# Performance work log

Measured on AMD Instinct MI355X. Metric: run time of the kernel, lower is better.

## Reference

```python
import jax, jax.numpy as jnp
import numpy as np

THRESHOLD = 1.0

@jax.custom_vjp
def spike(u):
    # Heaviside fire with snntorch ATan surrogate gradient (alpha=2.0)
    return (u > 0).astype(u.dtype)

def _spike_fwd(u):
    return spike(u), u

def _spike_bwd(u, g):
    # d/du atan surrogate: (alpha/2) / (1 + (pi/2*alpha*u)^2) with alpha=2 -> 1/(1+(pi*u)^2)
    return (g / (1.0 + (jnp.pi * u) ** 2),)

spike.defvjp(_spike_fwd, _spike_bwd)


def setup_inputs() -> dict:
    key = jax.random.key(0)
    k1, k2, k3, k4 = jax.random.split(key, 4)
    B, D, M = 1024, 256, 256
    x = jax.random.normal(k1, (B, D), dtype=jnp.float32)
    mem_states = jax.random.normal(k2, (M, B, D), dtype=jnp.float32)
    # mode_selector Linear(D -> M)
    W = jax.random.normal(k3, (M, D), dtype=jnp.float32) / np.sqrt(D)
    b = jax.random.normal(k4, (M,), dtype=jnp.float32) * 0.01
    return {"x": x, "mem_states": mem_states, "W": W, "b": b}


def reference(x, mem_states, W, b):
    M = mem_states.shape[0]
    # gating scores: [B, M]
    mode_scores = jax.nn.softmax(x @ W.T + b, axis=-1)
    # snn.Leaky(beta=i) for i in range(M): beta is the integer loop index
    betas = jnp.arange(M, dtype=x.dtype)[:, None, None]  # [M,1,1]
    # subtract-reset uses detached spike of the incoming membrane
    reset = jax.lax.stop_gradient((mem_states - THRESHOLD > 0).astype(x.dtype))
    mem_new = betas * mem_states + x[None, :, :] - reset * THRESHOLD  # [M,B,D]
    spk = spike(mem_new - THRESHOLD)  # [M,B,D]
    # faithful to source broadcast: [M,B,D] * [1,B,M] (requires D == M), sum over modes
    mixed = (spk * mode_scores[None, :, :]).sum(axis=0)  # [B,D]
    return mixed, mem_new, mode_scores
```

## Files before the change

### kernel.cpp

```cpp
#include <hip/hip_runtime.h>

#define THRESH 1.0f

typedef float fvec4 __attribute__((ext_vector_type(4)));

__global__ __launch_bounds__(256) void transpose_kernel(
    const float* __restrict__ W, float* __restrict__ Wt, int M, int D)
{
    __shared__ float tile[32][33];
    const int tilesK = D / 32;
    const int bx = blockIdx.x % tilesK;
    const int by = blockIdx.x / tilesK;
    const int lx = threadIdx.x & 31;
    const int ly = threadIdx.x >> 5;
    #pragma unroll
    for (int j = 0; j < 4; ++j)
        tile[ly + j * 8][lx] = W[(size_t)(by * 32 + ly + j * 8) * D + bx * 32 + lx];
    __syncthreads();
    #pragma unroll
    for (int j = 0; j < 4; ++j)
        Wt[(size_t)(bx * 32 + ly + j * 8) * M + by * 32 + lx] = tile[lx][ly + j * 8];
}

__global__ __launch_bounds__(256) void mega_kernel(
    const float* __restrict__ x, const float* __restrict__ mem,
    const float* __restrict__ Wt, const float* __restrict__ bias,
    float* __restrict__ mem_new, float* __restrict__ scores,
    float* __restrict__ mixed, int plane4)
{
    const int b    = blockIdx.x;
    const int tid  = threadIdx.x;
    const int wave = tid >> 6;
    const int lane = tid & 63;

    __shared__ __align__(16) float x_lds[256];
    __shared__ fvec4 sc_lds[64];
    __shared__ fvec4 cnt_lds[4][64];

    x_lds[tid] = x[(size_t)b * 256 + tid];
    __syncthreads();

    if (wave == 0) {
        const fvec4* Wt4 = reinterpret_cast<const fvec4*>(Wt);
        fvec4 acc = {0.f, 0.f, 0.f, 0.f};
        #pragma unroll 4
        for (int k = 0; k < 256; ++k) {
            const fvec4 w = Wt4[(size_t)k * 64 + lane];
            const float xk = x_lds[k];
            acc.x = fmaf(w.x, xk, acc.x);
            acc.y = fmaf(w.y, xk, acc.y);
            acc.z = fmaf(w.z, xk, acc.z);
            acc.w = fmaf(w.w, xk, acc.w);
        }
        const fvec4 bv = reinterpret_cast<const fvec4*>(bias)[lane];
        fvec4 lg;
        lg.x = acc.x + bv.x; lg.y = acc.y + bv.y;
        lg.z = acc.z + bv.z; lg.w = acc.w + bv.w;

        float mx = fmaxf(fmaxf(lg.x, lg.y), fmaxf(lg.z, lg.w));
        #pragma unroll
        for (int off = 32; off; off >>= 1) mx = fmaxf(mx, __shfl_xor(mx, off, 64));

        fvec4 e;
        e.x = expf(lg.x - mx); e.y = expf(lg.y - mx);
        e.z = expf(lg.z - mx); e.w = expf(lg.w - mx);
        float s = (e.x + e.y) + (e.z + e.w);
        #pragma unroll
        for (int off = 32; off; off >>= 1) s += __shfl_xor(s, off, 64);

        fvec4 sc;
        sc.x = e.x / s; sc.y = e.y / s; sc.z = e.z / s; sc.w = e.w / s;
        sc_lds[lane] = sc;
        reinterpret_cast<fvec4*>(scores)[(size_t)b * 64 + lane] = sc;
    }

    const int idx4 = b * 64 + lane;
    const fvec4 xv = reinterpret_cast<const fvec4*>(x_lds)[lane];
    const fvec4* mem4 = reinterpret_cast<const fvec4*>(mem);
    fvec4* out4       = reinterpret_cast<fvec4*>(mem_new);

    float cx = 0.f, cy = 0.f, cz = 0.f, cw = 0.f;
    const int m0 = wave * 64;

    #pragma unroll 4
    for (int j = 0; j < 64; ++j) {
        const int m = m0 + j;
        const float bm = (float)m;
        const size_t off = (size_t)m * plane4 + idx4;
        const fvec4 mv = __builtin_nontemporal_load(&mem4[off]);

        fvec4 nv;
        nv.x = __fsub_rn(__fadd_rn(__fmul_rn(bm, mv.x), xv.x),
                         (mv.x - THRESH > 0.f) ? THRESH : 0.f);
        nv.y = __fsub_rn(__fadd_rn(__fmul_rn(bm, mv.y), xv.y),
                         (mv.y - THRESH > 0.f) ? THRESH : 0.f);
        nv.z = __fsub_rn(__fadd_rn(__fmul_rn(bm, mv.z), xv.z),
                         (mv.z - THRESH > 0.f) ? THRESH : 0.f);
        nv.w = __fsub_rn(__fadd_rn(__fmul_rn(bm, mv.w), xv.w),
                         (mv.w - THRESH > 0.f) ? THRESH : 0.f);

        __builtin_nontemporal_store(nv, &out4[off]);

        cx += (nv.x - THRESH > 0.f) ? 1.f : 0.f;
        cy += (nv.y - THRESH > 0.f) ? 1.f : 0.f;
        cz += (nv.z - THRESH > 0.f) ? 1.f : 0.f;
        cw += (nv.w - THRESH > 0.f) ? 1.f : 0.f;
    }
    fvec4 cv; cv.x = cx; cv.y = cy; cv.z = cz; cv.w = cw;
    cnt_lds[wave][lane] = cv;
    __syncthreads();

    if (wave == 0) {
        const fvec4 c0 = cnt_lds[0][lane];
        const fvec4 c1 = cnt_lds[1][lane];
        const fvec4 c2 = cnt_lds[2][lane];
        const fvec4 c3 = cnt_lds[3][lane];
        fvec4 c;
        c.x = (c0.x + c1.x) + (c2.x + c3.x);
        c.y = (c0.y + c1.y) + (c2.y + c3.y);
        c.z = (c0.z + c1.z) + (c2.z + c3.z);
        c.w = (c0.w + c1.w) + (c2.w + c3.w);
        const fvec4 sc = sc_lds[lane];
        fvec4 r;
        r.x = sc.x * c.x; r.y = sc.y * c.y;
        r.z = sc.z * c.z; r.w = sc.w * c.w;
        reinterpret_cast<fvec4*>(mixed)[(size_t)idx4] = r;
    }
}

__global__ __launch_bounds__(256) void scores_kernel_fb(
    const float* __restrict__ x, const float* __restrict__ W,
    const float* __restrict__ bias, float* __restrict__ scores,
    int D, int M)
{
    const int b = blockIdx.x;
    __shared__ __align__(16) float x_lds[256];
    __shared__ float logits[256];
    __shared__ float wred[4];
    const int tid  = threadIdx.x;
    const int wave = tid >> 6;
    const int lane = tid & 63;
    x_lds[tid] = x[(size_t)b * D + tid];
    __syncthreads();
    const float4* W4 = reinterpret_cast<const float4*>(W);
    const float4  xv = reinterpret_cast<const float4*>(x_lds)[lane];
    for (int i = 0; i < 64; ++i) {
        const int m = wave * 64 + i;
        const float4 wv = W4[(size_t)m * 64 + lane];
        float p = wv.x * xv.x + wv.y * xv.y + wv.z * xv.z + wv.w * xv.w;
        #pragma unroll
        for (int off = 32; off; off >>= 1) p += __shfl_xor(p, off, 64);
        if (lane == 0) logits[m] = p + bias[m];
    }
    __syncthreads();
    float l = logits[tid];
    float mx = l;
    #pragma unroll
    for (int off = 32; off; off >>= 1) mx = fmaxf(mx, __shfl_xor(mx, off, 64));
    if (lane == 0) wred[wave] = mx;
    __syncthreads();
    mx = fmaxf(fmaxf(wred[0], wred[1]), fmaxf(wred[2], wred[3]));
    __syncthreads();
    const float e = expf(l - mx);
    float s = e;
    #pragma unroll
    for (int off = 32; off; off >>= 1) s += __shfl_xor(s, off, 64);
    if (lane == 0) wred[wave] = s;
    __syncthreads();
    const float tot = wred[0] + wred[1] + wred[2] + wred[3];
    scores[(size_t)b * M + tid] = e / tot;
}

__global__ __launch_bounds__(256) void neuron_kernel_fb(
    const float* __restrict__ x, const float* __restrict__ mem,
    const float* __restrict__ scores, float* __restrict__ mixed,
    float* __restrict__ mem_new, int M, int plane4)
{
    const int idx = blockIdx.x * 256 + threadIdx.x;
    if (idx >= plane4) return;
    const float4* x4   = reinterpret_cast<const float4*>(x);
    const float4* mem4 = reinterpret_cast<const float4*>(mem);
    const float4* sc4  = reinterpret_cast<const float4*>(scores);
    float4* out4       = reinterpret_cast<float4*>(mem_new);
    float4* mix4       = reinterpret_cast<float4*>(mixed);
    const float4 xv = x4[idx];
    float cx = 0.f, cy = 0.f, cz = 0.f, cw = 0.f;
    #pragma unroll 4
    for (int m = 0; m < M; ++m) {
        const float bm = (float)m;
        const size_t off = (size_t)m * plane4 + idx;
        const float4 mv = mem4[off];
        float4 nv;
        nv.x = __fsub_rn(__fadd_rn(__fmul_rn(bm, mv.x), xv.x),
                         (mv.x - THRESH > 0.f) ? THRESH : 0.f);
        nv.y = __fsub_rn(__fadd_rn(__fmul_rn(bm, mv.y), xv.y),
                         (mv.y - THRESH > 0.f) ? THRESH : 0.f);
        nv.z = __fsub_rn(__fadd_rn(__fmul_rn(bm, mv.z), xv.z),
                         (mv.z - THRESH > 0.f) ? THRESH : 0.f);
        nv.w = __fsub_rn(__fadd_rn(__fmul_rn(bm, mv.w), xv.w),
                         (mv.w - THRESH > 0.f) ? THRESH : 0.f);
        out4[off] = nv;
        cx += (nv.x - THRESH > 0.f) ? 1.f : 0.f;
        cy += (nv.y - THRESH > 0.f) ? 1.f : 0.f;
        cz += (nv.z - THRESH > 0.f) ? 1.f : 0.f;
        cw += (nv.w - THRESH > 0.f) ? 1.f : 0.f;
    }
    const float4 sc = sc4[idx];
    float4 mx;
    mx.x = sc.x * cx; mx.y = sc.y * cy; mx.z = sc.z * cz; mx.w = sc.w * cw;
    mix4[idx] = mx;
}

extern "C" void kernel_launch(void* const* d_in, const int* in_sizes, int n_in,
                              void* d_out, int out_size, void* d_ws, size_t ws_size,
                              hipStream_t stream) {
    const float* x    = (const float*)d_in[0];
    const float* mem  = (const float*)d_in[1];
    const float* W    = (const float*)d_in[2];
    const float* bias = (const float*)d_in[3];

    const int M = in_sizes[3];
    const int D = in_sizes[2] / M;
    const int B = in_sizes[0] / D;
    const int plane  = B * D;
    const int plane4 = plane / 4;

    float* out_mixed  = (float*)d_out;
    float* out_mem    = out_mixed + plane;
    float* out_scores = out_mem + (size_t)M * plane;

    const size_t wt_bytes = (size_t)M * D * sizeof(float);

    const bool shapes_ok = (D == 256) && (M == 256);

    if (shapes_ok && ws_size >= wt_bytes) {
        float* Wt = (float*)d_ws;
        transpose_kernel<<<(M / 32) * (D / 32), 256, 0, stream>>>(W, Wt, M, D);
        mega_kernel<<<B, 256, 0, stream>>>(
            x, mem, Wt, bias, out_mem, out_scores, out_mixed, plane4);
    } else {
        scores_kernel_fb<<<B, 256, 0, stream>>>(x, W, bias, out_scores, D, M);
        neuron_kernel_fb<<<(plane4 + 255) / 256, 256, 0, stream>>>(
            x, mem, out_scores, out_mixed, out_mem, M, plane4);
    }
}
```

Baseline: 111.7 us.

## Process two batch rows per block and spread scores GEMV across all waves

Each block now handles two batch rows, with all 256 threads computing one logit each for both rows. Each W element loaded is reused for two rows, and x values are broadcast through readlane instead of LDS. This replaces the single-wave GEMV that left three waves idle. The streaming loop is split into two halves of 128 modes over 128 float4 positions, which halves the grid and lengthens each thread's loop. The costs are fewer blocks (512), an extra block-level softmax reduction with syncs, and a changed fallback grid size.

```diff
diff --git a/kernel.cpp b/kernel.cpp
--- a/kernel.cpp
+++ b/kernel.cpp
@@ -3,6 +3,10 @@
 #define THRESH 1.0f
 
 typedef float fvec4 __attribute__((ext_vector_type(4)));
+
+__device__ __forceinline__ float rl(float v, int l) {
+    return __int_as_float(__builtin_amdgcn_readlane(__float_as_int(v), l));
+}
 
 __global__ __launch_bounds__(256) void transpose_kernel(
     const float* __restrict__ W, float* __restrict__ Wt, int M, int D)
@@ -22,71 +26,89 @@
         Wt[(size_t)(bx * 32 + ly + j * 8) * M + by * 32 + lx] = tile[lx][ly + j * 8];
 }
 
-__global__ __launch_bounds__(256) void mega_kernel(
+__global__ __launch_bounds__(256) void rowpair_kernel(
     const float* __restrict__ x, const float* __restrict__ mem,
     const float* __restrict__ Wt, const float* __restrict__ bias,
     float* __restrict__ mem_new, float* __restrict__ scores,
     float* __restrict__ mixed, int plane4)
 {
-    const int b    = blockIdx.x;
+    const int b0   = blockIdx.x * 2;
     const int tid  = threadIdx.x;
     const int wave = tid >> 6;
     const int lane = tid & 63;
 
-    __shared__ __align__(16) float x_lds[256];
-    __shared__ fvec4 sc_lds[64];
-    __shared__ fvec4 cnt_lds[4][64];
-
-    x_lds[tid] = x[(size_t)b * 256 + tid];
-    __syncthreads();
-
-    if (wave == 0) {
-        const fvec4* Wt4 = reinterpret_cast<const fvec4*>(Wt);
-        fvec4 acc = {0.f, 0.f, 0.f, 0.f};
-        #pragma unroll 4
-        for (int k = 0; k < 256; ++k) {
-            const fvec4 w = Wt4[(size_t)k * 64 + lane];
-            const float xk = x_lds[k];
-            acc.x = fmaf(w.x, xk, acc.x);
-            acc.y = fmaf(w.y, xk, acc.y);
-            acc.z = fmaf(w.z, xk, acc.z);
-            acc.w = fmaf(w.w, xk, acc.w);
-        }
-        const fvec4 bv = reinterpret_cast<const fvec4*>(bias)[lane];
-        fvec4 lg;
-        lg.x = acc.x + bv.x; lg.y = acc.y + bv.y;
-        lg.z = acc.z + bv.z; lg.w = acc.w + bv.w;
-
-        float mx = fmaxf(fmaxf(lg.x, lg.y), fmaxf(lg.z, lg.w));
-        #pragma unroll
-        for (int off = 32; off; off >>= 1) mx = fmaxf(mx, __shfl_xor(mx, off, 64));
-
-        fvec4 e;
-        e.x = expf(lg.x - mx); e.y = expf(lg.y - mx);
-        e.z = expf(lg.z - mx); e.w = expf(lg.w - mx);
-        float s = (e.x + e.y) + (e.z + e.w);
-        #pragma unroll
-        for (int off = 32; off; off >>= 1) s += __shfl_xor(s, off, 64);
-
-        fvec4 sc;
-        sc.x = e.x / s; sc.y = e.y / s; sc.z = e.z / s; sc.w = e.w / s;
-        sc_lds[lane] = sc;
-        reinterpret_cast<fvec4*>(scores)[(size_t)b * 64 + lane] = sc;
-    }
-
-    const int idx4 = b * 64 + lane;
-    const fvec4 xv = reinterpret_cast<const fvec4*>(x_lds)[lane];
+    __shared__ __align__(16) float sc_lds[2][256];
+    __shared__ fvec4 cnt_lds[2][128];
+    __shared__ float wredm[2][4];
+    __shared__ float wreds[2][4];
+
+    const fvec4 xq0 = reinterpret_cast<const fvec4*>(x)[(size_t)b0 * 64 + lane];
+    const fvec4 xq1 = reinterpret_cast<const fvec4*>(x)[(size_t)(b0 + 1) * 64 + lane];
+
+    float a0 = 0.f, a1 = 0.f;
+    #pragma unroll 4
+    for (int j = 0; j < 64; ++j) {
+        const float w0 = Wt[(size_t)(4 * j + 0) * 256 + tid];
+        const float w1 = Wt[(size_t)(4 * j + 1) * 256 + tid];
+        const float w2 = Wt[(size_t)(4 * j + 2) * 256 + tid];
+        const float w3 = Wt[(size_t)(4 * j + 3) * 256 + tid];
+        a0 = fmaf(w0, rl(xq0.x, j), a0);
+        a0 = fmaf(w1, rl(xq0.y, j), a0);
+        a0 = fmaf(w2, rl(xq0.z, j), a0);
+        a0 = fmaf(w3, rl(xq0.w, j), a0);
+        a1 = fmaf(w0, rl(xq1.x, j), a1);
+        a1 = fmaf(w1, rl(xq1.y, j), a1);
+        a1 = fmaf(w2, rl(xq1.z, j), a1);
+        a1 = fmaf(w3, rl(xq1.w, j), a1);
+    }
+    const float bv = bias[tid];
+    const float l0 = a0 + bv, l1 = a1 + bv;
+
+    float m0 = l0, m1 = l1;
+    #pragma unroll
+    for (int off = 32; off; off >>= 1) {
+        m0 = fmaxf(m0, __shfl_xor(m0, off, 64));
+        m1 = fmaxf(m1, __shfl_xor(m1, off, 64));
+    }
+    if (lane == 0) { wredm[0][wave] = m0; wredm[1][wave] = m1; }
+    __syncthreads();
+    m0 = fmaxf(fmaxf(wredm[0][0], wredm[0][1]), fmaxf(wredm[0][2], wredm[0][3]));
+    m1 = fmaxf(fmaxf(wredm[1][0], wredm[1][1]), fmaxf(wredm[1][2], wredm[1][3]));
+
+    const float e0 = expf(l0 - m0), e1 = expf(l1 - m1);
+    float s0 = e0, s1 = e1;
+    #pragma unroll
+    for (int off = 32; off; off >>= 1) {
+        s0 += __shfl_xor(s0, off, 64);
+        s1 += __shfl_xor(s1, off, 64);
+    }
+    if (lane == 0) { wreds[0][wave] = s0; wreds[1][wave] = s1; }
+    __syncthreads();
+    const float t0 = wreds[0][0] + wreds[0][1] + wreds[0][2] + wreds[0][3];
+    const float t1 = wreds[1][0] + wreds[1][1] + wreds[1][2] + wreds[1][3];
+
+    const float sc0 = e0 / t0, sc1 = e1 / t1;
+    sc_lds[0][tid] = sc0;
+    sc_lds[1][tid] = sc1;
+    scores[(size_t)b0 * 256 + tid]       = sc0;
+    scores[(size_t)(b0 + 1) * 256 + tid] = sc1;
+
+    const int h = tid >> 7;
+    const int p = tid & 127;
+    const int pos4 = b0 * 64 + p;
+    const fvec4 xv = reinterpret_cast<const fvec4*>(x)[pos4];
+
     const fvec4* mem4 = reinterpret_cast<const fvec4*>(mem);
     fvec4* out4       = reinterpret_cast<fvec4*>(mem_new);
 
     float cx = 0.f, cy = 0.f, cz = 0.f, cw = 0.f;
-    const int m0 = wave * 64;
-
-    #pragma unroll 4
-    for (int j = 0; j < 64; ++j) {
-        const int m = m0 + j;
+    const int mstart = h * 128;
+
+    #pragma unroll 8
+    for (int mm = 0; mm < 128; ++mm) {
+        const int m = mstart + mm;
         const float bm = (float)m;
-        const size_t off = (size_t)m * plane4 + idx4;
+        const size_t off = (size_t)m * plane4 + pos4;
         const fvec4 mv = __builtin_nontemporal_load(&mem4[off]);
 
         fvec4 nv;
@@ -107,24 +129,19 @@
         cw += (nv.w - THRESH > 0.f) ? 1.f : 0.f;
     }
     fvec4 cv; cv.x = cx; cv.y = cy; cv.z = cz; cv.w = cw;
-    cnt_lds[wave][lane] = cv;
-    __syncthreads();
-
-    if (wave == 0) {
-        const fvec4 c0 = cnt_lds[0][lane];
-        const fvec4 c1 = cnt_lds[1][lane];
-        const fvec4 c2 = cnt_lds[2][lane];
-        const fvec4 c3 = cnt_lds[3][lane];
-        fvec4 c;
-        c.x = (c0.x + c1.x) + (c2.x + c3.x);
-        c.y = (c0.y + c1.y) + (c2.y + c3.y);
-        c.z = (c0.z + c1.z) + (c2.z + c3.z);
-        c.w = (c0.w + c1.w) + (c2.w + c3.w);
-        const fvec4 sc = sc_lds[lane];
+    cnt_lds[h][p] = cv;
+    __syncthreads();
+
+    if (h == 0) {
+        const fvec4 cA = cnt_lds[0][p];
+        const fvec4 cB = cnt_lds[1][p];
+        const fvec4 sc = reinterpret_cast<const fvec4*>(sc_lds[p >> 6])[p & 63];
         fvec4 r;
-        r.x = sc.x * c.x; r.y = sc.y * c.y;
-        r.z = sc.z * c.z; r.w = sc.w * c.w;
-        reinterpret_cast<fvec4*>(mixed)[(size_t)idx4] = r;
+        r.x = sc.x * (cA.x + cB.x);
+        r.y = sc.y * (cA.y + cB.y);
+        r.z = sc.z * (cA.z + cB.z);
+        r.w = sc.w * (cA.w + cB.w);
+        reinterpret_cast<fvec4*>(mixed)[pos4] = r;
     }
 }
 
@@ -231,16 +248,16 @@
 
     const size_t wt_bytes = (size_t)M * D * sizeof(float);
 
-    const bool shapes_ok = (D == 256) && (M == 256);
+    const bool shapes_ok = (D == 256) && (M == 256) && (B % 2 == 0);
 
     if (shapes_ok && ws_size >= wt_bytes) {
         float* Wt = (float*)d_ws;
         transpose_kernel<<<(M / 32) * (D / 32), 256, 0, stream>>>(W, Wt, M, D);
-        mega_kernel<<<B, 256, 0, stream>>>(
+        rowpair_kernel<<<B / 2, 256, 0, stream>>>(
             x, mem, Wt, bias, out_mem, out_scores, out_mixed, plane4);
     } else {
         scores_kernel_fb<<<B, 256, 0, stream>>>(x, W, bias, out_scores, D, M);
-        neuron_kernel_fb<<<(plane4 + 255) / 256, 256, 0, stream>>>(
+        neuron_kernel_fb<<<(plane + 255) / 256 / 4, 256, 0, stream>>>(
             x, mem, out_scores, out_mixed, out_mem, M, plane4);
     }
 }
```

Measured after the change: 106.7 us. 1.05x faster.

## Spread gating GEMV across all waves and stagger it against streaming loop

Applied to the files above, without the earlier changes.

The softmax gating matvec, previously computed by a single wave while the other three waited, is now split so every thread computes one logit, using readlane broadcasts of x and block-wide max/sum reductions. Alternating groups of blocks run this prologue either before the mem_states stream or halfway through it, so compute phases in different blocks interleave with memory traffic. The goal is to shorten the serial compute head and overlap it with bandwidth-bound streaming. The cost is extra block-wide barriers in the middle of the streaming loop and a larger unroll, which may raise register pressure.

```diff
diff --git a/kernel.cpp b/kernel.cpp
--- a/kernel.cpp
+++ b/kernel.cpp
@@ -3,6 +3,10 @@
 #define THRESH 1.0f
 
 typedef float fvec4 __attribute__((ext_vector_type(4)));
+
+__device__ __forceinline__ float rl(float v, int l) {
+    return __int_as_float(__builtin_amdgcn_readlane(__float_as_int(v), l));
+}
 
 __global__ __launch_bounds__(256) void transpose_kernel(
     const float* __restrict__ W, float* __restrict__ Wt, int M, int D)
@@ -22,7 +26,7 @@
         Wt[(size_t)(bx * 32 + ly + j * 8) * M + by * 32 + lx] = tile[lx][ly + j * 8];
 }
 
-__global__ __launch_bounds__(256) void mega_kernel(
+__global__ __launch_bounds__(256) void row_kernel(
     const float* __restrict__ x, const float* __restrict__ mem,
     const float* __restrict__ Wt, const float* __restrict__ bias,
     float* __restrict__ mem_new, float* __restrict__ scores,
@@ -32,63 +36,25 @@
     const int tid  = threadIdx.x;
     const int wave = tid >> 6;
     const int lane = tid & 63;
-
-    __shared__ __align__(16) float x_lds[256];
-    __shared__ fvec4 sc_lds[64];
+    const int q    = wave;
+    const int p    = lane;
+    const int pos4 = b * 64 + p;
+
+    __shared__ __align__(16) float sc_f[256];
     __shared__ fvec4 cnt_lds[4][64];
-
-    x_lds[tid] = x[(size_t)b * 256 + tid];
-    __syncthreads();
-
-    if (wave == 0) {
-        const fvec4* Wt4 = reinterpret_cast<const fvec4*>(Wt);
-        fvec4 acc = {0.f, 0.f, 0.f, 0.f};
-        #pragma unroll 4
-        for (int k = 0; k < 256; ++k) {
-            const fvec4 w = Wt4[(size_t)k * 64 + lane];
-            const float xk = x_lds[k];
-            acc.x = fmaf(w.x, xk, acc.x);
-            acc.y = fmaf(w.y, xk, acc.y);
-            acc.z = fmaf(w.z, xk, acc.z);
-            acc.w = fmaf(w.w, xk, acc.w);
-        }
-        const fvec4 bv = reinterpret_cast<const fvec4*>(bias)[lane];
-        fvec4 lg;
-        lg.x = acc.x + bv.x; lg.y = acc.y + bv.y;
-        lg.z = acc.z + bv.z; lg.w = acc.w + bv.w;
-
-        float mx = fmaxf(fmaxf(lg.x, lg.y), fmaxf(lg.z, lg.w));
-        #pragma unroll
-        for (int off = 32; off; off >>= 1) mx = fmaxf(mx, __shfl_xor(mx, off, 64));
-
-        fvec4 e;
-        e.x = expf(lg.x - mx); e.y = expf(lg.y - mx);
-        e.z = expf(lg.z - mx); e.w = expf(lg.w - mx);
-        float s = (e.x + e.y) + (e.z + e.w);
-        #pragma unroll
-        for (int off = 32; off; off >>= 1) s += __shfl_xor(s, off, 64);
-
-        fvec4 sc;
-        sc.x = e.x / s; sc.y = e.y / s; sc.z = e.z / s; sc.w = e.w / s;
-        sc_lds[lane] = sc;
-        reinterpret_cast<fvec4*>(scores)[(size_t)b * 64 + lane] = sc;
-    }
-
-    const int idx4 = b * 64 + lane;
-    const fvec4 xv = reinterpret_cast<const fvec4*>(x_lds)[lane];
+    __shared__ float wredm[4];
+    __shared__ float wreds[4];
+
     const fvec4* mem4 = reinterpret_cast<const fvec4*>(mem);
     fvec4* out4       = reinterpret_cast<fvec4*>(mem_new);
+    const fvec4 xv    = reinterpret_cast<const fvec4*>(x)[pos4];
 
     float cx = 0.f, cy = 0.f, cz = 0.f, cw = 0.f;
-    const int m0 = wave * 64;
-
-    #pragma unroll 4
-    for (int j = 0; j < 64; ++j) {
-        const int m = m0 + j;
+
+    auto step = [&](int m) {
         const float bm = (float)m;
-        const size_t off = (size_t)m * plane4 + idx4;
+        const size_t off = (size_t)m * plane4 + pos4;
         const fvec4 mv = __builtin_nontemporal_load(&mem4[off]);
-
         fvec4 nv;
         nv.x = __fsub_rn(__fadd_rn(__fmul_rn(bm, mv.x), xv.x),
                          (mv.x - THRESH > 0.f) ? THRESH : 0.f);
@@ -98,33 +64,82 @@
                          (mv.z - THRESH > 0.f) ? THRESH : 0.f);
         nv.w = __fsub_rn(__fadd_rn(__fmul_rn(bm, mv.w), xv.w),
                          (mv.w - THRESH > 0.f) ? THRESH : 0.f);
-
         __builtin_nontemporal_store(nv, &out4[off]);
-
         cx += (nv.x - THRESH > 0.f) ? 1.f : 0.f;
         cy += (nv.y - THRESH > 0.f) ? 1.f : 0.f;
         cz += (nv.z - THRESH > 0.f) ? 1.f : 0.f;
         cw += (nv.w - THRESH > 0.f) ? 1.f : 0.f;
-    }
+    };
+
+    auto prologue = [&]() {
+        const fvec4 xq = reinterpret_cast<const fvec4*>(x)[(size_t)b * 64 + lane];
+        float a0 = 0.f;
+        #pragma unroll 4
+        for (int j = 0; j < 64; ++j) {
+            const float w0 = Wt[(size_t)(4 * j + 0) * 256 + tid];
+            const float w1 = Wt[(size_t)(4 * j + 1) * 256 + tid];
+            const float w2 = Wt[(size_t)(4 * j + 2) * 256 + tid];
+            const float w3 = Wt[(size_t)(4 * j + 3) * 256 + tid];
+            a0 = fmaf(w0, rl(xq.x, j), a0);
+            a0 = fmaf(w1, rl(xq.y, j), a0);
+            a0 = fmaf(w2, rl(xq.z, j), a0);
+            a0 = fmaf(w3, rl(xq.w, j), a0);
+        }
+        const float l = a0 + bias[tid];
+
+        float mx = l;
+        #pragma unroll
+        for (int off = 32; off; off >>= 1) mx = fmaxf(mx, __shfl_xor(mx, off, 64));
+        if (lane == 0) wredm[wave] = mx;
+        __syncthreads();
+        mx = fmaxf(fmaxf(wredm[0], wredm[1]), fmaxf(wredm[2], wredm[3]));
+
+        const float e = expf(l - mx);
+        float s = e;
+        #pragma unroll
+        for (int off = 32; off; off >>= 1) s += __shfl_xor(s, off, 64);
+        if (lane == 0) wreds[wave] = s;
+        __syncthreads();
+        const float tot = wreds[0] + wreds[1] + wreds[2] + wreds[3];
+
+        const float sc = e / tot;
+        sc_f[tid] = sc;
+        scores[(size_t)b * 256 + tid] = sc;
+    };
+
+    const int mstart = q * 64;
+
+    if (((blockIdx.x >> 3) & 1) == 0) {
+        #pragma unroll 8
+        for (int m = mstart; m < mstart + 32; ++m) step(m);
+        prologue();
+        #pragma unroll 8
+        for (int m = mstart + 32; m < mstart + 64; ++m) step(m);
+    } else {
+        prologue();
+        #pragma unroll 8
+        for (int m = mstart; m < mstart + 64; ++m) step(m);
+    }
+
     fvec4 cv; cv.x = cx; cv.y = cy; cv.z = cz; cv.w = cw;
-    cnt_lds[wave][lane] = cv;
-    __syncthreads();
-
-    if (wave == 0) {
-        const fvec4 c0 = cnt_lds[0][lane];
-        const fvec4 c1 = cnt_lds[1][lane];
-        const fvec4 c2 = cnt_lds[2][lane];
-        const fvec4 c3 = cnt_lds[3][lane];
+    cnt_lds[q][p] = cv;
+    __syncthreads();
+
+    if (q == 0) {
+        const fvec4 c0 = cnt_lds[0][p];
+        const fvec4 c1 = cnt_lds[1][p];
+        const fvec4 c2 = cnt_lds[2][p];
+        const fvec4 c3 = cnt_lds[3][p];
         fvec4 c;
         c.x = (c0.x + c1.x) + (c2.x + c3.x);
         c.y = (c0.y + c1.y) + (c2.y + c3.y);
         c.z = (c0.z + c1.z) + (c2.z + c3.z);
         c.w = (c0.w + c1.w) + (c2.w + c3.w);
-        const fvec4 sc = sc_lds[lane];
+        const fvec4 sc = reinterpret_cast<const fvec4*>(sc_f)[p];
         fvec4 r;
         r.x = sc.x * c.x; r.y = sc.y * c.y;
         r.z = sc.z * c.z; r.w = sc.w * c.w;
-        reinterpret_cast<fvec4*>(mixed)[(size_t)idx4] = r;
+        reinterpret_cast<fvec4*>(mixed)[pos4] = r;
     }
 }
 
@@ -147,10 +162,10 @@
     for (int i = 0; i < 64; ++i) {
         const int m = wave * 64 + i;
         const float4 wv = W4[(size_t)m * 64 + lane];
-        float p = wv.x * xv.x + wv.y * xv.y + wv.z * xv.z + wv.w * xv.w;
+        float pp = wv.x * xv.x + wv.y * xv.y + wv.z * xv.z + wv.w * xv.w;
         #pragma unroll
-        for (int off = 32; off; off >>= 1) p += __shfl_xor(p, off, 64);
-        if (lane == 0) logits[m] = p + bias[m];
+        for (int off = 32; off; off >>= 1) pp += __shfl_xor(pp, off, 64);
+        if (lane == 0) logits[m] = pp + bias[m];
     }
     __syncthreads();
     float l = logits[tid];
@@ -236,7 +251,7 @@
     if (shapes_ok && ws_size >= wt_bytes) {
         float* Wt = (float*)d_ws;
         transpose_kernel<<<(M / 32) * (D / 32), 256, 0, stream>>>(W, Wt, M, D);
-        mega_kernel<<<B, 256, 0, stream>>>(
+        row_kernel<<<B, 256, 0, stream>>>(
             x, mem, Wt, bias, out_mem, out_scores, out_mixed, plane4);
     } else {
         scores_kernel_fb<<<B, 256, 0, stream>>>(x, W, bias, out_scores, D, M);
```

Result: slower. 121.5 us (+8.8%).

## Process two batch rows per 512-thread block with uneven mode split

Applied to the files above, without the earlier changes.

Replaces the one-row-per-block kernel with a 512-thread block that handles two batch rows. Two waves compute the gating softmax, one per row, broadcasting x with readlane instead of staging it in LDS. Four thread groups split the 256 modes into uneven ranges (46/70/70/70), so the group that also did the GEMV gets fewer modes. The aim is to balance the GEMV work against the streaming loop and to halve the number of blocks and barriers, at the cost of more registers per block and a hardcoded partition.

```diff
diff --git a/kernel.cpp b/kernel.cpp
--- a/kernel.cpp
+++ b/kernel.cpp
@@ -3,6 +3,10 @@
 #define THRESH 1.0f
 
 typedef float fvec4 __attribute__((ext_vector_type(4)));
+
+__device__ __forceinline__ float rl(float v, int l) {
+    return __int_as_float(__builtin_amdgcn_readlane(__float_as_int(v), l));
+}
 
 __global__ __launch_bounds__(256) void transpose_kernel(
     const float* __restrict__ W, float* __restrict__ Wt, int M, int D)
@@ -22,35 +26,58 @@
         Wt[(size_t)(bx * 32 + ly + j * 8) * M + by * 32 + lx] = tile[lx][ly + j * 8];
 }
 
-__global__ __launch_bounds__(256) void mega_kernel(
+__global__ __launch_bounds__(512, 4) void rowpair512b_kernel(
     const float* __restrict__ x, const float* __restrict__ mem,
     const float* __restrict__ Wt, const float* __restrict__ bias,
     float* __restrict__ mem_new, float* __restrict__ scores,
     float* __restrict__ mixed, int plane4)
 {
-    const int b    = blockIdx.x;
+    const int b0   = blockIdx.x * 2;
     const int tid  = threadIdx.x;
     const int wave = tid >> 6;
     const int lane = tid & 63;
-
-    __shared__ __align__(16) float x_lds[256];
-    __shared__ fvec4 sc_lds[64];
-    __shared__ fvec4 cnt_lds[4][64];
-
-    x_lds[tid] = x[(size_t)b * 256 + tid];
-    __syncthreads();
-
-    if (wave == 0) {
+    const int q    = tid >> 7;
+    const int pp   = tid & 127;
+    const int pos4 = b0 * 64 + pp;
+
+    __shared__ fvec4 sc_lds[2][64];
+    __shared__ fvec4 cnt_lds[4][128];
+
+    const fvec4* mem4 = reinterpret_cast<const fvec4*>(mem);
+    fvec4* out4       = reinterpret_cast<fvec4*>(mem_new);
+    const fvec4* x4   = reinterpret_cast<const fvec4*>(x);
+
+    if (wave < 2) {
+        const int row = b0 + wave;
         const fvec4* Wt4 = reinterpret_cast<const fvec4*>(Wt);
+        const fvec4 xq = x4[(size_t)row * 64 + lane];
         fvec4 acc = {0.f, 0.f, 0.f, 0.f};
         #pragma unroll 4
-        for (int k = 0; k < 256; ++k) {
-            const fvec4 w = Wt4[(size_t)k * 64 + lane];
-            const float xk = x_lds[k];
-            acc.x = fmaf(w.x, xk, acc.x);
-            acc.y = fmaf(w.y, xk, acc.y);
-            acc.z = fmaf(w.z, xk, acc.z);
-            acc.w = fmaf(w.w, xk, acc.w);
+        for (int j = 0; j < 64; ++j) {
+            const float xk0 = rl(xq.x, j);
+            const float xk1 = rl(xq.y, j);
+            const float xk2 = rl(xq.z, j);
+            const float xk3 = rl(xq.w, j);
+            const fvec4 w0 = Wt4[(size_t)(4 * j + 0) * 64 + lane];
+            const fvec4 w1 = Wt4[(size_t)(4 * j + 1) * 64 + lane];
+            const fvec4 w2 = Wt4[(size_t)(4 * j + 2) * 64 + lane];
+            const fvec4 w3 = Wt4[(size_t)(4 * j + 3) * 64 + lane];
+            acc.x = fmaf(w0.x, xk0, acc.x);
+            acc.y = fmaf(w0.y, xk0, acc.y);
+            acc.z = fmaf(w0.z, xk0, acc.z);
+            acc.w = fmaf(w0.w, xk0, acc.w);
+            acc.x = fmaf(w1.x, xk1, acc.x);
+            acc.y = fmaf(w1.y, xk1, acc.y);
+            acc.z = fmaf(w1.z, xk1, acc.z);
+            acc.w = fmaf(w1.w, xk1, acc.w);
+            acc.x = fmaf(w2.x, xk2, acc.x);
+            acc.y = fmaf(w2.y, xk2, acc.y);
+            acc.z = fmaf(w2.z, xk2, acc.z);
+            acc.w = fmaf(w2.w, xk2, acc.w);
+            acc.x = fmaf(w3.x, xk3, acc.x);
+            acc.y = fmaf(w3.y, xk3, acc.y);
+            acc.z = fmaf(w3.z, xk3, acc.z);
+            acc.w = fmaf(w3.w, xk3, acc.w);
         }
         const fvec4 bv = reinterpret_cast<const fvec4*>(bias)[lane];
         fvec4 lg;
@@ -70,25 +97,21 @@
 
         fvec4 sc;
         sc.x = e.x / s; sc.y = e.y / s; sc.z = e.z / s; sc.w = e.w / s;
-        sc_lds[lane] = sc;
-        reinterpret_cast<fvec4*>(scores)[(size_t)b * 64 + lane] = sc;
-    }
-
-    const int idx4 = b * 64 + lane;
-    const fvec4 xv = reinterpret_cast<const fvec4*>(x_lds)[lane];
-    const fvec4* mem4 = reinterpret_cast<const fvec4*>(mem);
-    fvec4* out4       = reinterpret_cast<fvec4*>(mem_new);
-
+        sc_lds[wave][lane] = sc;
+        reinterpret_cast<fvec4*>(scores)[(size_t)row * 64 + lane] = sc;
+    }
+
+    const int MB[5] = {0, 46, 116, 186, 256};
+    const int m0 = MB[q], m1 = MB[q + 1];
+
+    const fvec4 xv = x4[pos4];
     float cx = 0.f, cy = 0.f, cz = 0.f, cw = 0.f;
-    const int m0 = wave * 64;
 
     #pragma unroll 4
-    for (int j = 0; j < 64; ++j) {
-        const int m = m0 + j;
+    for (int m = m0; m < m1; ++m) {
         const float bm = (float)m;
-        const size_t off = (size_t)m * plane4 + idx4;
+        const size_t off = (size_t)m * plane4 + pos4;
         const fvec4 mv = __builtin_nontemporal_load(&mem4[off]);
-
         fvec4 nv;
         nv.x = __fsub_rn(__fadd_rn(__fmul_rn(bm, mv.x), xv.x),
                          (mv.x - THRESH > 0.f) ? THRESH : 0.f);
@@ -98,33 +121,32 @@
                          (mv.z - THRESH > 0.f) ? THRESH : 0.f);
         nv.w = __fsub_rn(__fadd_rn(__fmul_rn(bm, mv.w), xv.w),
                          (mv.w - THRESH > 0.f) ? THRESH : 0.f);
-
         __builtin_nontemporal_store(nv, &out4[off]);
-
         cx += (nv.x - THRESH > 0.f) ? 1.f : 0.f;
         cy += (nv.y - THRESH > 0.f) ? 1.f : 0.f;
         cz += (nv.z - THRESH > 0.f) ? 1.f : 0.f;
         cw += (nv.w - THRESH > 0.f) ? 1.f : 0.f;
     }
+
     fvec4 cv; cv.x = cx; cv.y = cy; cv.z = cz; cv.w = cw;
-    cnt_lds[wave][lane] = cv;
-    __syncthreads();
-
-    if (wave == 0) {
-        const fvec4 c0 = cnt_lds[0][lane];
-        const fvec4 c1 = cnt_lds[1][lane];
-        const fvec4 c2 = cnt_lds[2][lane];
-        const fvec4 c3 = cnt_lds[3][lane];
+    cnt_lds[q][pp] = cv;
+    __syncthreads();
+
+    if (q == 0) {
+        const fvec4 c0 = cnt_lds[0][pp];
+        const fvec4 c1 = cnt_lds[1][pp];
+        const fvec4 c2 = cnt_lds[2][pp];
+        const fvec4 c3 = cnt_lds[3][pp];
         fvec4 c;
         c.x = (c0.x + c1.x) + (c2.x + c3.x);
         c.y = (c0.y + c1.y) + (c2.y + c3.y);
         c.z = (c0.z + c1.z) + (c2.z + c3.z);
         c.w = (c0.w + c1.w) + (c2.w + c3.w);
-        const fvec4 sc = sc_lds[lane];
+        const fvec4 sc = sc_lds[pp >> 6][pp & 63];
         fvec4 r;
         r.x = sc.x * c.x; r.y = sc.y * c.y;
         r.z = sc.z * c.z; r.w = sc.w * c.w;
-        reinterpret_cast<fvec4*>(mixed)[(size_t)idx4] = r;
+        reinterpret_cast<fvec4*>(mixed)[pos4] = r;
     }
 }
 
@@ -147,10 +169,10 @@
     for (int i = 0; i < 64; ++i) {
         const int m = wave * 64 + i;
         const float4 wv = W4[(size_t)m * 64 + lane];
-        float p = wv.x * xv.x + wv.y * xv.y + wv.z * xv.z + wv.w * xv.w;
+        float pp = wv.x * xv.x + wv.y * xv.y + wv.z * xv.z + wv.w * xv.w;
         #pragma unroll
-        for (int off = 32; off; off >>= 1) p += __shfl_xor(p, off, 64);
-        if (lane == 0) logits[m] = p + bias[m];
+        for (int off = 32; off; off >>= 1) pp += __shfl_xor(pp, off, 64);
+        if (lane == 0) logits[m] = pp + bias[m];
     }
     __syncthreads();
     float l = logits[tid];
@@ -231,12 +253,12 @@
 
     const size_t wt_bytes = (size_t)M * D * sizeof(float);
 
-    const bool shapes_ok = (D == 256) && (M == 256);
+    const bool shapes_ok = (D == 256) && (M == 256) && (B % 2 == 0);
 
     if (shapes_ok && ws_size >= wt_bytes) {
         float* Wt = (float*)d_ws;
         transpose_kernel<<<(M / 32) * (D / 32), 256, 0, stream>>>(W, Wt, M, D);
-        mega_kernel<<<B, 256, 0, stream>>>(
+        rowpair512b_kernel<<<B / 2, 512, 0, stream>>>(
             x, mem, Wt, bias, out_mem, out_scores, out_mixed, plane4);
     } else {
         scores_kernel_fb<<<B, 256, 0, stream>>>(x, W, bias, out_scores, D, M);
```

Result: no change. 110.2 us (-1.3%).
